# Optimization experiments

Hardware: AMD Instinct MI355X
Metric: run time of the kernel (lower is better)

Reference implementation:

```python
import jax, jax.numpy as jnp
import numpy as np

CHANNELS_CHOICE = np.array([8, 16, 24, 32, 40, 48, 56, 64])
MAX_C = 64
B, H, W_SP = 128, 32, 32
N_EDGES = 6
# edge list per intermediate node: (edge_weight_index, source_node_index)
EDGES = [[(0, 0)], [(1, 0), (2, 1)], [(3, 0), (4, 1), (5, 2)]]


def setup_inputs() -> dict:
    key = jax.random.key(0)
    k1, k2, k3, k4 = jax.random.split(key, 4)
    inputs = jax.random.normal(k1, (B, MAX_C, H, W_SP), dtype=jnp.float32)
    alphas1 = jax.random.uniform(k2, (8,), dtype=jnp.float32)  # input-width arch weights
    alphas2 = jax.random.uniform(k3, (8,), dtype=jnp.float32)  # output-width arch weights
    # shared master 3x3 conv weight per edge (OIHW)
    W = jax.random.normal(k4, (N_EDGES, MAX_C, MAX_C, 3, 3), dtype=jnp.float32) * 0.05
    return {"inputs": inputs, "alphas1": alphas1, "alphas2": alphas2, "W": W}


def _channel_scale(alphas1, alphas2, dtype):
    # mask[c, i] = 1 if channel c is inside width choice CHANNELS_CHOICE[i]
    mask = (jnp.arange(MAX_C)[:, None] < jnp.asarray(CHANNELS_CHOICE)[None, :]).astype(dtype)  # [64, 8]
    a_in = mask @ alphas1   # [64] cumulative input-channel weight
    a_out = mask @ alphas2  # [64] cumulative output-channel weight
    return a_out[:, None] * a_in[None, :]  # [64, 64]


def _edge(x, w, scale):
    # weighted-combi of all (c1, c2) channel-sliced sub-convs == one conv with scaled weight
    w_eff = w * scale[:, :, None, None]
    return jax.lax.conv_general_dilated(
        jax.nn.relu(x), w_eff, window_strides=(1, 1), padding="SAME",
        dimension_numbers=("NCHW", "OIHW", "NCHW"))


def reference(inputs, alphas1, alphas2, W):
    scale = _channel_scale(alphas1, alphas2, inputs.dtype)
    nodes = [inputs]
    for node_edges in EDGES:
        feat = 0.0
        for l, src in node_edges:
            feat = feat + _edge(nodes[src], W[l], scale)
        nodes.append(feat)
    return nodes[-1]
```

## Files before the change

### kernel.cpp

```cpp
#include <hip/hip_runtime.h>
#include <hip/hip_bf16.h>


typedef __bf16 bf16x8 __attribute__((ext_vector_type(8)));
typedef float floatx4 __attribute__((ext_vector_type(4)));
typedef unsigned int uint32;

#define PADW 34
#define PIMG (PADW * PADW)
#define ROWB (PADW * 64 * 2)
#define A_LDS (18 * ROWB)
#define A_CHUNKS (A_LDS / 16)
#define TAPB (64 * 64 * 2)
#define B_LDS (9 * TAPB)
#define B_CHUNKS (B_LDS / 16)
#define SMEM_BYTES (A_LDS + B_LDS)

__device__ __forceinline__ void gld16(const char* g, char* l) {
    __builtin_amdgcn_global_load_lds(
        (const __attribute__((address_space(1))) uint32*)g,
        (__attribute__((address_space(3))) uint32*)l, 16, 0, 0);
}

__global__ __launch_bounds__(256) void pre_kernel(
    const float* __restrict__ in, const float* __restrict__ a1,
    const float* __restrict__ a2, const float* __restrict__ W,
    __hip_bfloat16* __restrict__ wt, __hip_bfloat16* __restrict__ r0,
    __hip_bfloat16* __restrict__ r1, __hip_bfloat16* __restrict__ r2) {
    __shared__ float tile[32][65];
    int blk = blockIdx.x;
    int tid = threadIdx.x;

    if (blk < 864) {
        int idx = blk * 256 + tid;
        int i = idx & 63;
        int o = (idx >> 6) & 63;
        int rest = idx >> 12;
        int t = rest % 9;
        int l = rest / 9;
        int ji = i >> 3, jo = o >> 3;
        float ain = 0.f, aout = 0.f;
#pragma unroll
        for (int j = 0; j < 8; ++j) {
            ain  += (j >= ji) ? a1[j] : 0.f;
            aout += (j >= jo) ? a2[j] : 0.f;
        }
        float v = W[(size_t)((l * 64 + o) * 64 + i) * 9 + t] * ain * aout;
        size_t e = (size_t)(l * 9 + t) * 4096 + o * 64 +
                   ((((i >> 3) ^ (o & 7)) << 3) + (i & 7));
        wt[e] = __float2bfloat16(v);
    } else if (blk < 992) {
        int b = blk - 864;
        __hip_bfloat16* bufs[3] = {r0, r1, r2};
#pragma unroll
        for (int f = 0; f < 3; ++f) {
            uint32* buf = (uint32*)(bufs[f] + (size_t)b * PIMG * 64);
            for (int idx = tid; idx < 132 * 32; idx += 256) {
                int slot = idx >> 5, u = idx & 31;
                int yy, xx;
                if (slot < 34)      { yy = 0;  xx = slot; }
                else if (slot < 68) { yy = 33; xx = slot - 34; }
                else { int s2 = slot - 68; yy = 1 + (s2 >> 1); xx = (s2 & 1) * 33; }
                buf[(size_t)(yy * PADW + xx) * 32 + u] = 0u;
            }
        }
    } else {
        int rb = blk - 992;
        int b = rb >> 5, y = rb & 31;
        int x = tid & 31, c0 = tid >> 5;
        const float* ip = in + ((size_t)b * 64 * 32 + y) * 32 + x;
#pragma unroll
        for (int cc = 0; cc < 8; ++cc) {
            int c = cc * 8 + c0;
            tile[x][c] = fmaxf(ip[(size_t)c * 1024], 0.f);
        }
        __syncthreads();
        int o = tid & 63, xg = tid >> 6;
        int p0 = (b * PADW + y + 1) * PADW + 1;
#pragma unroll
        for (int xx = 0; xx < 8; ++xx) {
            int xq = xx * 4 + xg;
            int p = p0 + xq;
            size_t e = (size_t)p * 64 + ((((o >> 3) ^ (p & 7)) << 3) + (o & 7));
            r0[e] = __float2bfloat16(tile[xq][o]);
        }
    }
}

template <int NSRC, bool FINAL>
__global__ __launch_bounds__(512, 2) void conv_stage(
    const __hip_bfloat16* __restrict__ s0,
    const __hip_bfloat16* __restrict__ s1,
    const __hip_bfloat16* __restrict__ s2,
    const __hip_bfloat16* __restrict__ wt,
    void* __restrict__ dstv, int l0) {
    extern __shared__ char smem[];
    char* smemB = smem + A_LDS;
    int tid = threadIdx.x;
    int wv = tid >> 6, lane = tid & 63;
    int quad = lane >> 4, l15 = lane & 15;
    int blk = blockIdx.x;
    int b = blk >> 1, y0 = (blk & 1) << 4;

    const char* srcs[3] = {(const char*)s0, (const char*)s1, (const char*)s2};
    const char* gW = (const char*)wt + (size_t)l0 * 9 * (size_t)TAPB;

    auto stage_A = [&](int s) {
        const char* gA = srcs[s] + (size_t)(b * PADW + y0) * PADW * 128;
#pragma unroll
        for (int it = 0; it < 10; ++it) {
            int c = it * 512 + tid;
            if (it < 9 || tid < A_CHUNKS - 9 * 512)
                gld16(gA + (size_t)c * 16, smem + (it * 512 + wv * 64) * 16);
        }
    };
    auto stage_B = [&](int s) {
        const char* gB = gW + (size_t)s * 9 * TAPB;
#pragma unroll
        for (int it = 0; it < 9; ++it) {
            int c = it * 512 + tid;
            gld16(gB + (size_t)c * 16, smemB + (it * 512 + wv * 64) * 16);
        }
    };

    floatx4 acc[4][4];
#pragma unroll
    for (int m = 0; m < 4; ++m)
#pragma unroll
        for (int n = 0; n < 4; ++n) acc[m][n] = (floatx4){0.f, 0.f, 0.f, 0.f};

    stage_A(0);
    stage_B(0);
    __syncthreads();

#pragma unroll 1
    for (int s = 0; s < NSRC; ++s) {
#pragma unroll
        for (int tl = 0; tl < 9; ++tl) {
            const int ky = tl / 3, kx = tl % 3;
#pragma unroll
            for (int q = 0; q < 2; ++q) {
                bf16x8 Af[4], Bf[4];
#pragma unroll
                for (int m = 0; m < 4; ++m) {
                    int arow = 2 * wv + (m >> 1) + ky;
                    int apx  = ((m & 1) << 4) + l15 + kx;
                    int R = b * PADW + y0 + arow;
                    int slot = ((q << 2) + quad) ^ ((2 * R + apx) & 7);
                    Af[m] = *(const bf16x8*)(smem + arow * ROWB +
                                             apx * 128 + slot * 16);
                }
#pragma unroll
                for (int n = 0; n < 4; ++n) {
                    int o = (n << 4) + l15;
                    int slot = ((q << 2) + quad) ^ (l15 & 7);
                    Bf[n] = *(const bf16x8*)(smemB + tl * TAPB +
                                             o * 128 + slot * 16);
                }
#pragma unroll
                for (int m = 0; m < 4; ++m)
#pragma unroll
                    for (int n = 0; n < 4; ++n)
                        acc[m][n] = __builtin_amdgcn_mfma_f32_16x16x32_bf16(
                            Af[m], Bf[n], acc[m][n], 0, 0, 0);
            }
        }
        if (s + 1 < NSRC) {
            __syncthreads();
            stage_A(s + 1);
            stage_B(s + 1);
            __syncthreads();
        }
    }

    if (FINAL) {
        float* out = (float*)dstv;
#pragma unroll
        for (int m = 0; m < 4; ++m) {
            int row = y0 + 2 * wv + (m >> 1);
#pragma unroll
            for (int n = 0; n < 4; ++n) {
                int o = (n << 4) + l15;
                *(floatx4*)(out + (((size_t)b * 64 + o) * 32 + row) * 32 +
                            ((m & 1) << 4) + (quad << 2)) = acc[m][n];
            }
        }
    } else {
        __hip_bfloat16* out = (__hip_bfloat16*)dstv;
#pragma unroll
        for (int m = 0; m < 4; ++m) {
            int row = y0 + 2 * wv + (m >> 1);
#pragma unroll
            for (int n = 0; n < 4; ++n) {
                int o = (n << 4) + l15;
#pragma unroll
                for (int r = 0; r < 4; ++r) {
                    int x = ((m & 1) << 4) + (quad << 2) + r;
                    int p = (b * PADW + row + 1) * PADW + x + 1;
                    float v = fmaxf(acc[m][n][r], 0.f);
                    size_t e = (size_t)p * 64 +
                               ((((o >> 3) ^ (p & 7)) << 3) + (o & 7));
                    out[e] = __float2bfloat16(v);
                }
            }
        }
    }
}

extern "C" void kernel_launch(void* const* d_in, const int* in_sizes, int n_in,
                              void* d_out, int out_size, void* d_ws,
                              size_t ws_size, hipStream_t stream) {
    const float* inputs  = (const float*)d_in[0];
    const float* alphas1 = (const float*)d_in[1];
    const float* alphas2 = (const float*)d_in[2];
    const float* W       = (const float*)d_in[3];
    char* ws = (char*)d_ws;

    __hip_bfloat16* wt = (__hip_bfloat16*)(ws);
    __hip_bfloat16* r0 = (__hip_bfloat16*)(ws + ((size_t)1 << 20));
    __hip_bfloat16* r1 = (__hip_bfloat16*)(ws + ((size_t)20 << 20));
    __hip_bfloat16* r2 = (__hip_bfloat16*)(ws + ((size_t)40 << 20));
    float* out = (float*)d_out;

    (void)hipFuncSetAttribute((const void*)conv_stage<1, false>,
                              hipFuncAttributeMaxDynamicSharedMemorySize,
                              SMEM_BYTES);
    (void)hipFuncSetAttribute((const void*)conv_stage<2, false>,
                              hipFuncAttributeMaxDynamicSharedMemorySize,
                              SMEM_BYTES);
    (void)hipFuncSetAttribute((const void*)conv_stage<3, true>,
                              hipFuncAttributeMaxDynamicSharedMemorySize,
                              SMEM_BYTES);

    pre_kernel<<<864 + 128 + 4096, 256, 0, stream>>>(inputs, alphas1, alphas2,
                                                     W, wt, r0, r1, r2);
    conv_stage<1, false><<<256, 512, SMEM_BYTES, stream>>>(r0, r1, r2, wt,
                                                           (void*)r1, 0);
    conv_stage<2, false><<<256, 512, SMEM_BYTES, stream>>>(r0, r1, r2, wt,
                                                           (void*)r2, 1);
    conv_stage<3, true ><<<256, 512, SMEM_BYTES, stream>>>(r0, r1, r2, wt,
                                                           (void*)out, 3);
}
```

Baseline: 151.5 us.

## Prefetch next source into registers during MFMA loop and vectorize pre-kernel stores

```diff
diff --git a/kernel.cpp b/kernel.cpp
--- a/kernel.cpp
+++ b/kernel.cpp
@@ -11,6 +11,7 @@
 #define ROWB (PADW * 64 * 2)
 #define A_LDS (18 * ROWB)
 #define A_CHUNKS (A_LDS / 16)
+#define A_TAIL (A_CHUNKS - 9 * 512)
 #define TAPB (64 * 64 * 2)
 #define B_LDS (9 * TAPB)
 #define B_CHUNKS (B_LDS / 16)
@@ -75,15 +76,14 @@
             tile[x][c] = fmaxf(ip[(size_t)c * 1024], 0.f);
         }
         __syncthreads();
-        int o = tid & 63, xg = tid >> 6;
-        int p0 = (b * PADW + y + 1) * PADW + 1;
-#pragma unroll
-        for (int xx = 0; xx < 8; ++xx) {
-            int xq = xx * 4 + xg;
-            int p = p0 + xq;
-            size_t e = (size_t)p * 64 + ((((o >> 3) ^ (p & 7)) << 3) + (o & 7));
-            r0[e] = __float2bfloat16(tile[xq][o]);
-        }
+        int j = tid & 7, xq = tid >> 3;
+        int p = (b * PADW + y + 1) * PADW + 1 + xq;
+        alignas(16) __hip_bfloat16 hv[8];
+#pragma unroll
+        for (int k = 0; k < 8; ++k)
+            hv[k] = __float2bfloat16(tile[xq][j * 8 + k]);
+        *(uint4*)((char*)r0 + (size_t)p * 128 + ((j ^ (p & 7)) << 4)) =
+            *(const uint4*)hv;
     }
 }
 
@@ -110,7 +110,7 @@
 #pragma unroll
         for (int it = 0; it < 10; ++it) {
             int c = it * 512 + tid;
-            if (it < 9 || tid < A_CHUNKS - 9 * 512)
+            if (it < 9 || tid < A_TAIL)
                 gld16(gA + (size_t)c * 16, smem + (it * 512 + wv * 64) * 16);
         }
     };
@@ -123,6 +123,28 @@
         }
     };
 
+    uint4 pfA[10], pfB[9];
+    auto prefetch = [&](int s) {
+        const char* gA = srcs[s] + (size_t)(b * PADW + y0) * PADW * 128;
+#pragma unroll
+        for (int it = 0; it < 10; ++it)
+            if (it < 9 || tid < A_TAIL)
+                pfA[it] = *(const uint4*)(gA + (size_t)(it * 512 + tid) * 16);
+        const char* gB = gW + (size_t)s * 9 * TAPB;
+#pragma unroll
+        for (int it = 0; it < 9; ++it)
+            pfB[it] = *(const uint4*)(gB + (size_t)(it * 512 + tid) * 16);
+    };
+    auto commit = [&]() {
+#pragma unroll
+        for (int it = 0; it < 10; ++it)
+            if (it < 9 || tid < A_TAIL)
+                *(uint4*)(smem + (size_t)(it * 512 + tid) * 16) = pfA[it];
+#pragma unroll
+        for (int it = 0; it < 9; ++it)
+            *(uint4*)(smemB + (size_t)(it * 512 + tid) * 16) = pfB[it];
+    };
+
     floatx4 acc[4][4];
 #pragma unroll
     for (int m = 0; m < 4; ++m)
@@ -135,6 +157,10 @@
 
 #pragma unroll 1
     for (int s = 0; s < NSRC; ++s) {
+        if (s + 1 < NSRC) {
+            prefetch(s + 1);
+            __builtin_amdgcn_sched_barrier(0);
+        }
 #pragma unroll
         for (int tl = 0; tl < 9; ++tl) {
             const int ky = tl / 3, kx = tl % 3;
@@ -157,18 +183,19 @@
                     Bf[n] = *(const bf16x8*)(smemB + tl * TAPB +
                                              o * 128 + slot * 16);
                 }
+                __builtin_amdgcn_s_setprio(1);
 #pragma unroll
                 for (int m = 0; m < 4; ++m)
 #pragma unroll
                     for (int n = 0; n < 4; ++n)
                         acc[m][n] = __builtin_amdgcn_mfma_f32_16x16x32_bf16(
                             Af[m], Bf[n], acc[m][n], 0, 0, 0);
+                __builtin_amdgcn_s_setprio(0);
             }
         }
         if (s + 1 < NSRC) {
             __syncthreads();
-            stage_A(s + 1);
-            stage_B(s + 1);
+            commit();
             __syncthreads();
         }
     }
```

Result: slower. 189.3 us (+24.9%).

## Halve conv tile rows, double-buffer weight taps, vectorize relu-to-bf16 stores

Applied to the files above, without the earlier changes.

```diff
diff --git a/kernel.cpp b/kernel.cpp
--- a/kernel.cpp
+++ b/kernel.cpp
@@ -9,12 +9,12 @@
 #define PADW 34
 #define PIMG (PADW * PADW)
 #define ROWB (PADW * 64 * 2)
-#define A_LDS (18 * ROWB)
+#define A_LDS (10 * ROWB)
 #define A_CHUNKS (A_LDS / 16)
+#define A_TAIL (A_CHUNKS - 10 * 256)
 #define TAPB (64 * 64 * 2)
-#define B_LDS (9 * TAPB)
-#define B_CHUNKS (B_LDS / 16)
-#define SMEM_BYTES (A_LDS + B_LDS)
+#define GRPB (2 * TAPB)
+#define SMEM_BYTES (A_LDS + 2 * GRPB)
 
 __device__ __forceinline__ void gld16(const char* g, char* l) {
     __builtin_amdgcn_global_load_lds(
@@ -75,20 +75,19 @@
             tile[x][c] = fmaxf(ip[(size_t)c * 1024], 0.f);
         }
         __syncthreads();
-        int o = tid & 63, xg = tid >> 6;
-        int p0 = (b * PADW + y + 1) * PADW + 1;
-#pragma unroll
-        for (int xx = 0; xx < 8; ++xx) {
-            int xq = xx * 4 + xg;
-            int p = p0 + xq;
-            size_t e = (size_t)p * 64 + ((((o >> 3) ^ (p & 7)) << 3) + (o & 7));
-            r0[e] = __float2bfloat16(tile[xq][o]);
-        }
+        int j = tid & 7, xq = tid >> 3;
+        int p = (b * PADW + y + 1) * PADW + 1 + xq;
+        alignas(16) __hip_bfloat16 hv[8];
+#pragma unroll
+        for (int k = 0; k < 8; ++k)
+            hv[k] = __float2bfloat16(tile[xq][j * 8 + k]);
+        *(uint4*)((char*)r0 + (size_t)p * 128 + ((j ^ (p & 7)) << 4)) =
+            *(const uint4*)hv;
     }
 }
 
 template <int NSRC, bool FINAL>
-__global__ __launch_bounds__(512, 2) void conv_stage(
+__global__ __launch_bounds__(256, 2) void conv_stage(
     const __hip_bfloat16* __restrict__ s0,
     const __hip_bfloat16* __restrict__ s1,
     const __hip_bfloat16* __restrict__ s2,
@@ -100,7 +99,7 @@
     int wv = tid >> 6, lane = tid & 63;
     int quad = lane >> 4, l15 = lane & 15;
     int blk = blockIdx.x;
-    int b = blk >> 1, y0 = (blk & 1) << 4;
+    int b = blk >> 2, y0 = (blk & 3) << 3;
 
     const char* srcs[3] = {(const char*)s0, (const char*)s1, (const char*)s2};
     const char* gW = (const char*)wt + (size_t)l0 * 9 * (size_t)TAPB;
@@ -108,18 +107,18 @@
     auto stage_A = [&](int s) {
         const char* gA = srcs[s] + (size_t)(b * PADW + y0) * PADW * 128;
 #pragma unroll
-        for (int it = 0; it < 10; ++it) {
-            int c = it * 512 + tid;
-            if (it < 9 || tid < A_CHUNKS - 9 * 512)
-                gld16(gA + (size_t)c * 16, smem + (it * 512 + wv * 64) * 16);
+        for (int it = 0; it < 11; ++it) {
+            int c = it * 256 + tid;
+            if (it < 10 || tid < A_TAIL)
+                gld16(gA + (size_t)c * 16, smem + (it * 256 + wv * 64) * 16);
         }
     };
-    auto stage_B = [&](int s) {
-        const char* gB = gW + (size_t)s * 9 * TAPB;
-#pragma unroll
-        for (int it = 0; it < 9; ++it) {
-            int c = it * 512 + tid;
-            gld16(gB + (size_t)c * 16, smemB + (it * 512 + wv * 64) * 16);
+    auto stage_B = [&](int s, int tap0, int nt, char* dst) {
+#pragma unroll
+        for (int it = 0; it < 2 * nt; ++it) {
+            const char* gB = gW + ((size_t)s * 9 + tap0) * TAPB;
+            gld16(gB + (size_t)(it * 256 + tid) * 16,
+                  dst + (it * 256 + wv * 64) * 16);
         }
     };
 
@@ -130,46 +129,64 @@
         for (int n = 0; n < 4; ++n) acc[m][n] = (floatx4){0.f, 0.f, 0.f, 0.f};
 
     stage_A(0);
-    stage_B(0);
+    stage_B(0, 0, 2, smemB);
     __syncthreads();
 
 #pragma unroll 1
     for (int s = 0; s < NSRC; ++s) {
-#pragma unroll
-        for (int tl = 0; tl < 9; ++tl) {
-            const int ky = tl / 3, kx = tl % 3;
-#pragma unroll
-            for (int q = 0; q < 2; ++q) {
-                bf16x8 Af[4], Bf[4];
-#pragma unroll
-                for (int m = 0; m < 4; ++m) {
-                    int arow = 2 * wv + (m >> 1) + ky;
-                    int apx  = ((m & 1) << 4) + l15 + kx;
-                    int R = b * PADW + y0 + arow;
-                    int slot = ((q << 2) + quad) ^ ((2 * R + apx) & 7);
-                    Af[m] = *(const bf16x8*)(smem + arow * ROWB +
-                                             apx * 128 + slot * 16);
+        int sb = s & 1;
+#pragma unroll
+        for (int g = 0; g < 5; ++g) {
+            const int t0 = 2 * g;
+            const int GT = (g == 4) ? 1 : 2;
+            char* Bcur = smemB + (((g & 1) ? sb ^ 1 : sb) ? GRPB : 0);
+            char* Bnxt = smemB + (((g & 1) ? sb ^ 1 : sb) ? 0 : GRPB);
+            if (g < 4) {
+                const int nt0 = (g + 1 == 4) ? 1 : 2;
+                stage_B(s, 2 * (g + 1), nt0, Bnxt);
+            } else if (s + 1 < NSRC) {
+                stage_B(s + 1, 0, 2, Bnxt);
+            }
+            __builtin_amdgcn_sched_barrier(0);
+#pragma unroll
+            for (int tt = 0; tt < GT; ++tt) {
+                const int tl = t0 + tt, ky = tl / 3, kx = tl % 3;
+#pragma unroll
+                for (int q = 0; q < 2; ++q) {
+                    bf16x8 Af[4], Bf[4];
+#pragma unroll
+                    for (int m = 0; m < 4; ++m) {
+                        int arow = 2 * wv + (m >> 1) + ky;
+                        int apx  = ((m & 1) << 4) + l15 + kx;
+                        int R = b * PADW + y0 + arow;
+                        int slot = ((q << 2) + quad) ^ ((2 * R + apx) & 7);
+                        Af[m] = *(const bf16x8*)(smem + arow * ROWB +
+                                                 apx * 128 + slot * 16);
+                    }
+#pragma unroll
+                    for (int n = 0; n < 4; ++n) {
+                        int o = (n << 4) + l15;
+                        int slot = ((q << 2) + quad) ^ (l15 & 7);
+                        Bf[n] = *(const bf16x8*)(Bcur + tt * TAPB +
+                                                 o * 128 + slot * 16);
+                    }
+                    __builtin_amdgcn_s_setprio(1);
+#pragma unroll
+                    for (int m = 0; m < 4; ++m)
+#pragma unroll
+                        for (int n = 0; n < 4; ++n)
+                            acc[m][n] =
+                                __builtin_amdgcn_mfma_f32_16x16x32_bf16(
+                                    Af[m], Bf[n], acc[m][n], 0, 0, 0);
+                    __builtin_amdgcn_s_setprio(0);
                 }
-#pragma unroll
-                for (int n = 0; n < 4; ++n) {
-                    int o = (n << 4) + l15;
-                    int slot = ((q << 2) + quad) ^ (l15 & 7);
-                    Bf[n] = *(const bf16x8*)(smemB + tl * TAPB +
-                                             o * 128 + slot * 16);
-                }
-#pragma unroll
-                for (int m = 0; m < 4; ++m)
-#pragma unroll
-                    for (int n = 0; n < 4; ++n)
-                        acc[m][n] = __builtin_amdgcn_mfma_f32_16x16x32_bf16(
-                            Af[m], Bf[n], acc[m][n], 0, 0, 0);
-            }
-        }
-        if (s + 1 < NSRC) {
-            __syncthreads();
-            stage_A(s + 1);
-            stage_B(s + 1);
-            __syncthreads();
+            }
+            if (g < 4 || s + 1 < NSRC)
+                __syncthreads();
+            if (g == 4 && s + 1 < NSRC) {
+                stage_A(s + 1);
+                __syncthreads();
+            }
         }
     }
 
@@ -234,10 +251,10 @@
 
     pre_kernel<<<864 + 128 + 4096, 256, 0, stream>>>(inputs, alphas1, alphas2,
                                                      W, wt, r0, r1, r2);
-    conv_stage<1, false><<<256, 512, SMEM_BYTES, stream>>>(r0, r1, r2, wt,
+    conv_stage<1, false><<<512, 256, SMEM_BYTES, stream>>>(r0, r1, r2, wt,
                                                            (void*)r1, 0);
-    conv_stage<2, false><<<256, 512, SMEM_BYTES, stream>>>(r0, r1, r2, wt,
+    conv_stage<2, false><<<512, 256, SMEM_BYTES, stream>>>(r0, r1, r2, wt,
                                                            (void*)r2, 1);
-    conv_stage<3, true ><<<256, 512, SMEM_BYTES, stream>>>(r0, r1, r2, wt,
+    conv_stage<3, true ><<<512, 256, SMEM_BYTES, stream>>>(r0, r1, r2, wt,
                                                            (void*)out, 3);
 }
```

New measurement: 154.2 us. Within noise of the previous version (+1.8%).

## Load conv activations directly from global memory, shrink blocks, vectorize pre-store

Applied to the files above, without the earlier changes.

```diff
diff --git a/kernel.cpp b/kernel.cpp
--- a/kernel.cpp
+++ b/kernel.cpp
@@ -8,18 +8,19 @@
 
 #define PADW 34
 #define PIMG (PADW * PADW)
-#define ROWB (PADW * 64 * 2)
-#define A_LDS (18 * ROWB)
-#define A_CHUNKS (A_LDS / 16)
 #define TAPB (64 * 64 * 2)
 #define B_LDS (9 * TAPB)
 #define B_CHUNKS (B_LDS / 16)
-#define SMEM_BYTES (A_LDS + B_LDS)
+#define SMEM_BYTES B_LDS
 
 __device__ __forceinline__ void gld16(const char* g, char* l) {
     __builtin_amdgcn_global_load_lds(
         (const __attribute__((address_space(1))) uint32*)g,
         (__attribute__((address_space(3))) uint32*)l, 16, 0, 0);
+}
+
+__device__ __forceinline__ bf16x8 gload8(const char* g) {
+    return *(const __attribute__((address_space(1))) bf16x8*)g;
 }
 
 __global__ __launch_bounds__(256) void pre_kernel(
@@ -75,52 +76,41 @@
             tile[x][c] = fmaxf(ip[(size_t)c * 1024], 0.f);
         }
         __syncthreads();
-        int o = tid & 63, xg = tid >> 6;
-        int p0 = (b * PADW + y + 1) * PADW + 1;
-#pragma unroll
-        for (int xx = 0; xx < 8; ++xx) {
-            int xq = xx * 4 + xg;
-            int p = p0 + xq;
-            size_t e = (size_t)p * 64 + ((((o >> 3) ^ (p & 7)) << 3) + (o & 7));
-            r0[e] = __float2bfloat16(tile[xq][o]);
-        }
+        int j = tid & 7, xq = tid >> 3;
+        int p = (b * PADW + y + 1) * PADW + 1 + xq;
+        alignas(16) __hip_bfloat16 hv[8];
+#pragma unroll
+        for (int k = 0; k < 8; ++k)
+            hv[k] = __float2bfloat16(tile[xq][j * 8 + k]);
+        *(uint4*)((char*)r0 + (size_t)p * 128 + ((j ^ (p & 7)) << 4)) =
+            *(const uint4*)hv;
     }
 }
 
 template <int NSRC, bool FINAL>
-__global__ __launch_bounds__(512, 2) void conv_stage(
+__global__ __launch_bounds__(256, 2) void conv_stage(
     const __hip_bfloat16* __restrict__ s0,
     const __hip_bfloat16* __restrict__ s1,
     const __hip_bfloat16* __restrict__ s2,
     const __hip_bfloat16* __restrict__ wt,
     void* __restrict__ dstv, int l0) {
-    extern __shared__ char smem[];
-    char* smemB = smem + A_LDS;
+    extern __shared__ char smemB[];
     int tid = threadIdx.x;
     int wv = tid >> 6, lane = tid & 63;
     int quad = lane >> 4, l15 = lane & 15;
     int blk = blockIdx.x;
-    int b = blk >> 1, y0 = (blk & 1) << 4;
+    int b = blk >> 2, y0 = (blk & 3) << 3;
+    int Rb = b * PADW + y0;
 
     const char* srcs[3] = {(const char*)s0, (const char*)s1, (const char*)s2};
     const char* gW = (const char*)wt + (size_t)l0 * 9 * (size_t)TAPB;
 
-    auto stage_A = [&](int s) {
-        const char* gA = srcs[s] + (size_t)(b * PADW + y0) * PADW * 128;
-#pragma unroll
-        for (int it = 0; it < 10; ++it) {
-            int c = it * 512 + tid;
-            if (it < 9 || tid < A_CHUNKS - 9 * 512)
-                gld16(gA + (size_t)c * 16, smem + (it * 512 + wv * 64) * 16);
-        }
-    };
     auto stage_B = [&](int s) {
         const char* gB = gW + (size_t)s * 9 * TAPB;
 #pragma unroll
-        for (int it = 0; it < 9; ++it) {
-            int c = it * 512 + tid;
-            gld16(gB + (size_t)c * 16, smemB + (it * 512 + wv * 64) * 16);
-        }
+        for (int it = 0; it < 18; ++it)
+            gld16(gB + (size_t)(it * 256 + tid) * 16,
+                  smemB + (it * 256 + wv * 64) * 16);
     };
 
     floatx4 acc[4][4];
@@ -129,26 +119,32 @@
 #pragma unroll
         for (int n = 0; n < 4; ++n) acc[m][n] = (floatx4){0.f, 0.f, 0.f, 0.f};
 
-    stage_A(0);
     stage_B(0);
     __syncthreads();
 
 #pragma unroll 1
     for (int s = 0; s < NSRC; ++s) {
+        const char* gA = srcs[s];
 #pragma unroll
         for (int tl = 0; tl < 9; ++tl) {
             const int ky = tl / 3, kx = tl % 3;
+            size_t pp[4];
+            int p7[4];
+#pragma unroll
+            for (int m = 0; m < 4; ++m) {
+                int R = Rb + 2 * wv + (m >> 1) + ky;
+                int apx = ((m & 1) << 4) + l15 + kx;
+                int p = R * PADW + apx;
+                pp[m] = (size_t)p * 128;
+                p7[m] = p & 7;
+            }
 #pragma unroll
             for (int q = 0; q < 2; ++q) {
                 bf16x8 Af[4], Bf[4];
 #pragma unroll
                 for (int m = 0; m < 4; ++m) {
-                    int arow = 2 * wv + (m >> 1) + ky;
-                    int apx  = ((m & 1) << 4) + l15 + kx;
-                    int R = b * PADW + y0 + arow;
-                    int slot = ((q << 2) + quad) ^ ((2 * R + apx) & 7);
-                    Af[m] = *(const bf16x8*)(smem + arow * ROWB +
-                                             apx * 128 + slot * 16);
+                    int slot = ((q << 2) + quad) ^ p7[m];
+                    Af[m] = gload8(gA + pp[m] + slot * 16);
                 }
 #pragma unroll
                 for (int n = 0; n < 4; ++n) {
@@ -157,17 +153,18 @@
                     Bf[n] = *(const bf16x8*)(smemB + tl * TAPB +
                                              o * 128 + slot * 16);
                 }
+                __builtin_amdgcn_s_setprio(1);
 #pragma unroll
                 for (int m = 0; m < 4; ++m)
 #pragma unroll
                     for (int n = 0; n < 4; ++n)
                         acc[m][n] = __builtin_amdgcn_mfma_f32_16x16x32_bf16(
                             Af[m], Bf[n], acc[m][n], 0, 0, 0);
+                __builtin_amdgcn_s_setprio(0);
             }
         }
         if (s + 1 < NSRC) {
             __syncthreads();
-            stage_A(s + 1);
             stage_B(s + 1);
             __syncthreads();
         }
@@ -234,10 +231,10 @@
 
     pre_kernel<<<864 + 128 + 4096, 256, 0, stream>>>(inputs, alphas1, alphas2,
                                                      W, wt, r0, r1, r2);
-    conv_stage<1, false><<<256, 512, SMEM_BYTES, stream>>>(r0, r1, r2, wt,
+    conv_stage<1, false><<<512, 256, SMEM_BYTES, stream>>>(r0, r1, r2, wt,
                                                            (void*)r1, 0);
-    conv_stage<2, false><<<256, 512, SMEM_BYTES, stream>>>(r0, r1, r2, wt,
+    conv_stage<2, false><<<512, 256, SMEM_BYTES, stream>>>(r0, r1, r2, wt,
                                                            (void*)r2, 1);
-    conv_stage<3, true ><<<256, 512, SMEM_BYTES, stream>>>(r0, r1, r2, wt,
+    conv_stage<3, true ><<<512, 256, SMEM_BYTES, stream>>>(r0, r1, r2, wt,
                                                            (void*)out, 3);
 }
```

Measured after the change: 212.9 us. 40.5% more time.
